# Kernel tuning notes

Measured on AMD Instinct MI355X. Metric: run time of the kernel, lower is better.

## Reference

```python
import jax, jax.numpy as jnp
import numpy as np

H, N, CH = 256, 64, 1  # heads/features, diagonal state size, channels


def setup_inputs() -> dict:
    key = jax.random.key(0)
    k1, k2, k3 = jax.random.split(key, 3)
    # |A| in (0.5, 0.999) so exp(dtA * l) decays for large l (matches rho*w construction)
    A_abslog = jnp.log(jax.random.uniform(k1, (H, N), dtype=jnp.float32,
                                          minval=0.5, maxval=0.999))
    A_phase = jax.random.uniform(k2, (H, N), dtype=jnp.float32,
                                 minval=-np.pi, maxval=np.pi)
    # C stored as real view of complex (channels, H, N, 2), like torch.view_as_real
    C = jax.random.normal(k3, (CH, H, N, 2), dtype=jnp.float32)
    return {"A_abslog": A_abslog, "A_phase": A_phase, "C": C, "L": 4096}


def reference(A_abslog, A_phase, C, L):
    # A_eigvals = exp(abslog + i*phase), copies=1 so repeat is identity
    A = jnp.exp(A_abslog + 1j * A_phase)            # (H, N) complex64
    dtA = jnp.log(A)                                 # (H, N)
    Cc = C[..., 0] + 1j * C[..., 1]                  # (CH, H, N)
    Cc = Cc * (A - 1.0) / dtA                        # (CH, H, N)
    t = jnp.arange(L, dtype=jnp.float32)             # (L,)
    K = jnp.exp(dtA[:, :, None] * t)                 # (H, N, L) Vandermonde
    K = jnp.einsum('chn,hnl->chl', Cc, K)            # (CH, H, L)
    return 2.0 * K.real
```

## Files before the change

kernel.cpp:

```cpp
#include <hip/hip_runtime.h>
#include <math.h>


typedef float f32x2 __attribute__((ext_vector_type(2)));

constexpr int H = 256;
constexpr int N = 64;
constexpr int L = 4096;

constexpr int BLK   = 256;
constexpr int WAVES = 4;
constexpr int NPW   = N / WAVES;
constexpr int PPW   = NPW / 2;
constexpr int LPT   = 16;
constexpr int LBLK  = 64 * LPT;
constexpr int NP    = N / 2;
constexpr int RPAD  = LPT + 1;

__global__ __launch_bounds__(BLK, 4)
void sskdiag_kernel(const float* __restrict__ A_abslog,
                    const float* __restrict__ A_phase,
                    const float* __restrict__ C,
                    float* __restrict__ out)
{
    __shared__ float4 s_P[NP];
    __shared__ float4 s_Q[NP];
    __shared__ float4 s_CC[NP];
    __shared__ float4 s_alph[NP];
    __shared__ float  s_red[WAVES][64][RPAD];

    const int h     = blockIdx.x >> 2;
    const int lbase = (blockIdx.x & 3) * LBLK;
    const int tid   = threadIdx.x;
    const int w     = tid >> 6;
    const int lane  = tid & 63;

    if (tid < N) {
        const int   n  = tid;
        const float al = A_abslog[h * N + n];
        const float ph = A_phase [h * N + n];
        const double inv2pi = 0.15915494309189535;
        const double md = (double)ph * inv2pi;
        const float phrev = (float)(md - floor(md));
        const float sp = __builtin_amdgcn_sinf(phrev);
        const float cp = __builtin_amdgcn_cosf(phrev);
        const float m  = __expf(al);
        const float Ar = m * cp, Ai = m * sp;
        const float nr = Ar - 1.0f, ni = Ai;
        const float inv = 1.0f / (al * al + ph * ph);
        const float gr = (nr * al + ni * ph) * inv;
        const float gi = (ni * al - nr * ph) * inv;
        const float cre = C[(h * N + n) * 2 + 0];
        const float cim = C[(h * N + n) * 2 + 1];
        const float Cr = cre * gr - cim * gi;
        const float Ci = cre * gi + cim * gr;
        const float magP = __expf(al * (float)lbase);
        const double mdl = (double)ph * (double)lbase * inv2pi;
        const float  fl  = (float)(mdl - floor(mdl));
        const float er = magP * __builtin_amdgcn_cosf(fl);
        const float ei = magP * __builtin_amdgcn_sinf(fl);
        const float Pr = Cr * er - Ci * ei;
        const float Pi = Cr * ei + Ci * er;
        const float Qr = Pr * Ar - Pi * Ai;
        const float Qi = Pr * Ai + Pi * Ar;
        const int pr = n >> 1, sl = n & 1;
        ((float*)&s_P [pr])[sl]     = Pr;
        ((float*)&s_P [pr])[2 + sl] = -Pi;
        ((float*)&s_Q [pr])[sl]     = Qr;
        ((float*)&s_Q [pr])[2 + sl] = -Qi;
        ((float*)&s_CC[pr])[sl]     = Ar + Ar;
        ((float*)&s_CC[pr])[2 + sl] = -(Ar * Ar + Ai * Ai);
        ((float*)&s_alph[pr])[sl]     = al;
        ((float*)&s_alph[pr])[2 + sl] = phrev;
    }
    __syncthreads();

    const float kf = (float)(LPT * lane);

    f32x2 acc[LPT];
    #pragma unroll
    for (int j = 0; j < LPT; ++j) acc[j] = (f32x2){0.f, 0.f};

    #pragma unroll 2
    for (int p = 0; p < PPW; ++p) {
        const float4 ap = s_alph[PPW * w + p];
        const float m0 = __expf(ap.x * kf);
        const float m1 = __expf(ap.y * kf);
        float t0 = ap.z * kf; t0 -= floorf(t0);
        float t1 = ap.w * kf; t1 -= floorf(t1);
        const f32x2 TX = { m0 * __builtin_amdgcn_cosf(t0),
                           m1 * __builtin_amdgcn_cosf(t1) };
        const f32x2 TY = { m0 * __builtin_amdgcn_sinf(t0),
                           m1 * __builtin_amdgcn_sinf(t1) };

        const float4 P  = s_P [PPW * w + p];
        const float4 Q  = s_Q [PPW * w + p];
        const float4 CV = s_CC[PPW * w + p];
        const f32x2 PR = {P.x, P.y},  PI = {P.z, P.w};
        const f32x2 QR = {Q.x, Q.y},  QI = {Q.z, Q.w};
        const f32x2 C1 = {CV.x, CV.y}, C2 = {CV.z, CV.w};

        f32x2 rp = TX * PR + TY * PI;
        f32x2 rc = TX * QR + TY * QI;
        acc[0] += rp;
        acc[1] += rc;
        #pragma unroll
        for (int j = 2; j < LPT; ++j) {
            const f32x2 rn = C1 * rc + C2 * rp;
            acc[j] += rn;
            rp = rc; rc = rn;
        }
    }

    #pragma unroll
    for (int j = 0; j < LPT; ++j)
        s_red[w][lane][j] = acc[j].x + acc[j].y;
    __syncthreads();

    {
        const int lp = tid >> 2;
        const int j0 = (tid & 3) * 4;
        float s0 = 0.f, s1 = 0.f, s2 = 0.f, s3 = 0.f;
        #pragma unroll
        for (int ww = 0; ww < WAVES; ++ww) {
            s0 += s_red[ww][lp][j0 + 0];
            s1 += s_red[ww][lp][j0 + 1];
            s2 += s_red[ww][lp][j0 + 2];
            s3 += s_red[ww][lp][j0 + 3];
        }
        float4 v;
        v.x = 2.0f * s0;  v.y = 2.0f * s1;
        v.z = 2.0f * s2;  v.w = 2.0f * s3;
        *reinterpret_cast<float4*>(out + h * L + lbase + 4 * tid) = v;
    }
}

extern "C" void kernel_launch(void* const* d_in, const int* in_sizes, int n_in,
                              void* d_out, int out_size, void* d_ws, size_t ws_size,
                              hipStream_t stream)
{
    const float* A_abslog = (const float*)d_in[0];
    const float* A_phase  = (const float*)d_in[1];
    const float* C        = (const float*)d_in[2];
    float* out = (float*)d_out;

    sskdiag_kernel<<<H * (L / LBLK), BLK, 0, stream>>>(A_abslog, A_phase, C, out);
}
```

Measured before the change: 11.99 us.

## Halve per-thread recurrence length and double grid split along L

Each thread now runs an 8-step recurrence instead of 16, so each block covers 512 outputs and the grid has twice as many blocks per head. The launch bounds target higher occupancy. The reduction buffer is relaid out as float2 indexed [j][wave][lane] to give conflict-free shared-memory access, and the output store becomes float2. The block-offset phase is computed in float from the reduced phase, which drops the double-precision math but may lose accuracy at large offsets. The trade-off is more redundant per-block setup (exp and sincos per state) and more transcendental evaluations per output.

```diff
diff --git a/kernel.cpp b/kernel.cpp
--- a/kernel.cpp
+++ b/kernel.cpp
@@ -12,12 +12,12 @@
 constexpr int WAVES = 4;
 constexpr int NPW   = N / WAVES;
 constexpr int PPW   = NPW / 2;
-constexpr int LPT   = 16;
+constexpr int LPT   = 8;
 constexpr int LBLK  = 64 * LPT;
+constexpr int SPLIT = L / LBLK;
 constexpr int NP    = N / 2;
-constexpr int RPAD  = LPT + 1;
 
-__global__ __launch_bounds__(BLK, 4)
+__global__ __launch_bounds__(BLK, 8)
 void sskdiag_kernel(const float* __restrict__ A_abslog,
                     const float* __restrict__ A_phase,
                     const float* __restrict__ C,
@@ -27,10 +27,10 @@
     __shared__ float4 s_Q[NP];
     __shared__ float4 s_CC[NP];
     __shared__ float4 s_alph[NP];
-    __shared__ float  s_red[WAVES][64][RPAD];
+    __shared__ f32x2  s_red[LPT][WAVES][64];
 
-    const int h     = blockIdx.x >> 2;
-    const int lbase = (blockIdx.x & 3) * LBLK;
+    const int h     = blockIdx.x >> 3;
+    const int lbase = (blockIdx.x & 7) * LBLK;
     const int tid   = threadIdx.x;
     const int w     = tid >> 6;
     const int lane  = tid & 63;
@@ -39,8 +39,7 @@
         const int   n  = tid;
         const float al = A_abslog[h * N + n];
         const float ph = A_phase [h * N + n];
-        const double inv2pi = 0.15915494309189535;
-        const double md = (double)ph * inv2pi;
+        const double md = (double)ph * 0.15915494309189535;
         const float phrev = (float)(md - floor(md));
         const float sp = __builtin_amdgcn_sinf(phrev);
         const float cp = __builtin_amdgcn_cosf(phrev);
@@ -54,11 +53,11 @@
         const float cim = C[(h * N + n) * 2 + 1];
         const float Cr = cre * gr - cim * gi;
         const float Ci = cre * gi + cim * gr;
-        const float magP = __expf(al * (float)lbase);
-        const double mdl = (double)ph * (double)lbase * inv2pi;
-        const float  fl  = (float)(mdl - floor(mdl));
-        const float er = magP * __builtin_amdgcn_cosf(fl);
-        const float ei = magP * __builtin_amdgcn_sinf(fl);
+        const float lbf  = (float)lbase;
+        const float magP = __expf(al * lbf);
+        float tl = phrev * lbf;  tl -= floorf(tl);
+        const float er = magP * __builtin_amdgcn_cosf(tl);
+        const float ei = magP * __builtin_amdgcn_sinf(tl);
         const float Pr = Cr * er - Ci * ei;
         const float Pi = Cr * ei + Ci * er;
         const float Qr = Pr * Ar - Pi * Ai;
@@ -114,24 +113,22 @@
 
     #pragma unroll
     for (int j = 0; j < LPT; ++j)
-        s_red[w][lane][j] = acc[j].x + acc[j].y;
+        s_red[j][w][lane] = acc[j];
     __syncthreads();
 
     {
         const int lp = tid >> 2;
-        const int j0 = (tid & 3) * 4;
-        float s0 = 0.f, s1 = 0.f, s2 = 0.f, s3 = 0.f;
+        const int jb = (tid & 3) * 2;
+        f32x2 u0 = {0.f, 0.f}, u1 = {0.f, 0.f};
         #pragma unroll
         for (int ww = 0; ww < WAVES; ++ww) {
-            s0 += s_red[ww][lp][j0 + 0];
-            s1 += s_red[ww][lp][j0 + 1];
-            s2 += s_red[ww][lp][j0 + 2];
-            s3 += s_red[ww][lp][j0 + 3];
+            u0 += s_red[jb + 0][ww][lp];
+            u1 += s_red[jb + 1][ww][lp];
         }
-        float4 v;
-        v.x = 2.0f * s0;  v.y = 2.0f * s1;
-        v.z = 2.0f * s2;  v.w = 2.0f * s3;
-        *reinterpret_cast<float4*>(out + h * L + lbase + 4 * tid) = v;
+        float2 v;
+        v.x = 2.0f * (u0.x + u0.y);
+        v.y = 2.0f * (u1.x + u1.y);
+        *reinterpret_cast<float2*>(out + h * L + lbase + lp * LPT + jb) = v;
     }
 }
 
@@ -144,5 +141,5 @@
     const float* C        = (const float*)d_in[2];
     float* out = (float*)d_out;
 
-    sskdiag_kernel<<<H * (L / LBLK), BLK, 0, stream>>>(A_abslog, A_phase, C, out);
+    sskdiag_kernel<<<H * SPLIT, BLK, 0, stream>>>(A_abslog, A_phase, C, out);
 }
```

Result: slower. 13.41 us (+11.8%).
